# Optimization experiments

Hardware: AMD Instinct MI355X
Metric: run time of the kernel (lower is better)

## Reference

```python
import jax, jax.numpy as jnp
import numpy as np
import math

MODEL_DIM = 1024
BATCH = 4
SEQ = 2048


def setup_inputs() -> dict:
    key = jax.random.key(0)
    kx, kq, kk, kv = jax.random.split(key, 4)
    x = jax.random.normal(kx, (BATCH, SEQ, MODEL_DIM), dtype=jnp.float32)
    # kaiming_uniform_(W.T, a=sqrt(5)) on a square matrix -> U(-b, b) with
    # b = sqrt(6 / ((1 + 5) * fan_in)) = 1/sqrt(model_dim)
    bound = 1.0 / math.sqrt(MODEL_DIM)
    Q = jax.random.uniform(kq, (MODEL_DIM, MODEL_DIM), jnp.float32, -bound, bound)
    K = jax.random.uniform(kk, (MODEL_DIM, MODEL_DIM), jnp.float32, -bound, bound)
    V = jax.random.uniform(kv, (MODEL_DIM, MODEL_DIM), jnp.float32, -bound, bound)
    # attention_input='both' => a = model_dim => F is the full identity mask
    F = jnp.eye(MODEL_DIM, dtype=jnp.float32)
    return {"x": x, "F": F, "Q": Q, "K": K, "V": V}


def reference(x, F, Q, K, V):
    # Qx = x @ F @ Q ; Kx = x @ F @ K ; Vx = x @ V
    xF = x @ F                      # [b, s, d]
    Qx = xF @ Q                     # [b, s, d]
    Kx = xF @ K                     # [b, s, d]
    Vx = x @ V                      # [b, s, d]
    scale = 1.0 / math.sqrt(MODEL_DIM)
    attn_scores = jnp.einsum('bsd,btd->bst', Qx, Kx) * scale  # [b, s, s]
    attn_probs = jax.nn.softmax(attn_scores, axis=-1)
    out = jnp.einsum('bst,btd->bsd', attn_probs, Vx)          # [b, s, d]
    return out
```

## Files before the change

kernel.cpp:

```cpp
#include <hip/hip_runtime.h>
#include <hip/hip_bf16.h>

using bf16 = __hip_bfloat16;
typedef __bf16 bf16x8 __attribute__((ext_vector_type(8)));
typedef float f32x4 __attribute__((ext_vector_type(4)));
typedef float f32x16 __attribute__((ext_vector_type(16)));

#define AS3(p) ((__attribute__((address_space(3))) void*)(p))
#define AS1(p) ((const __attribute__((address_space(1))) void*)(p))

template <int W> __device__ __forceinline__ void waitv() {
  asm volatile("s_waitcnt vmcnt(%0)" ::"n"(W) : "memory");
}
#define BARR __builtin_amdgcn_s_barrier()
#define LGKM0 asm volatile("s_waitcnt lgkmcnt(0)" ::: "memory")
#define SCHEDB __builtin_amdgcn_sched_barrier(0)

__device__ __forceinline__ void swz_bid(int& bx, int& by, int& bz) {
  const int gx = gridDim.x, gy = gridDim.y;
  const int nwg = gx * gy * gridDim.z;
  const int l = blockIdx.x + gx * (blockIdx.y + gy * blockIdx.z);
  const int L = (l & 7) * (nwg >> 3) + (l >> 3);
  bx = L % gx;
  by = (L / gx) % gy;
  bz = L / (gx * gy);
}

__global__ void cast_f32_bf16_kernel(const float* __restrict__ in,
                                     bf16* __restrict__ out, int n4) {
  int i = blockIdx.x * blockDim.x + threadIdx.x;
  if (i >= n4) return;
  float4 v = reinterpret_cast<const float4*>(in)[i];
  union { ushort4 u; bf16 h[4]; } o;
  o.h[0] = __float2bfloat16(v.x);
  o.h[1] = __float2bfloat16(v.y);
  o.h[2] = __float2bfloat16(v.z);
  o.h[3] = __float2bfloat16(v.w);
  reinterpret_cast<ushort4*>(out)[i] = o.u;
}

__global__ void transpose3_kernel(const float* __restrict__ W0,
                                  const float* __restrict__ W1,
                                  const float* __restrict__ W2,
                                  bf16* __restrict__ out) {
  __shared__ bf16 tile[32][33];
  const float* in = (blockIdx.z == 0) ? W0 : (blockIdx.z == 1) ? W1 : W2;
  out += (long)blockIdx.z * 1024 * 1024;
  int c0 = blockIdx.x * 32, r0 = blockIdx.y * 32;
  for (int i = threadIdx.y; i < 32; i += 8)
    tile[i][threadIdx.x] = (bf16)in[(long)(r0 + i) * 1024 + c0 + threadIdx.x];
  __syncthreads();
  for (int i = threadIdx.y; i < 32; i += 8)
    out[(long)(c0 + i) * 1024 + r0 + threadIdx.x] = tile[threadIdx.x][i];
}

__device__ inline void store_c(float* p, float v) { *p = v; }
__device__ inline void store_c(bf16* p, float v) { *p = __float2bfloat16(v); }

template <int MODE, typename OutT>
__global__ __launch_bounds__(512, 1) void gemm8p_kernel(
    const bf16* __restrict__ A, const bf16* __restrict__ Bt, OutT* __restrict__ C,
    int K, int lda, int ldb, int ldc, long sAb, long sBb, long sCb,
    float* __restrict__ aux, int auxStride) {
  constexpr int HALF = 128 * 64;
  constexpr int BB = 4 * HALF;
  __shared__ alignas(16) bf16 lds[2 * BB];

  int bx, by, bz;
  swz_bid(bx, by, bz);
  A += (long)bz * sAb;
  Bt += (long)bz * sBb;
  C += (long)bz * sCb;
  if (MODE != 0) aux += (long)bz * auxStride;
  const int tm = by * 256, tn = bx * 256;
  const int tid = threadIdx.x, wv = tid >> 6, lane = tid & 63;
  const int wm = wv >> 2, wn = wv & 3;
  const int lrow = lane & 15, lkc = lane >> 4;

  f32x4 acc[8][4] = {};
  bf16x8 afr[4][2], bfr[2][2][2];

  const int co0 = (lkc ^ (lrow & 7)) * 8;
  const int co1 = ((4 + lkc) ^ (lrow & 7)) * 8;
  const int arow = wm * 64 + lrow;
  const int brow = wn * 32 + lrow;

  auto stageA = [&](bf16* buf, int kt, int mh) {
#pragma unroll
    for (int i = 0; i < 2; ++i) {
      int slot = i * 512 + tid;
      int rp = slot >> 3;
      int g = (rp & 63) | (mh << 6) | ((rp >> 6) << 7);
      int cg = (slot & 7) ^ (rp & 7);
      const bf16* src = A + (long)(tm + g) * lda + kt + cg * 8;
      __builtin_amdgcn_global_load_lds(AS1(src), AS3(buf + mh * HALF + slot * 8), 16, 0, 0);
    }
  };
  auto stageB = [&](bf16* buf, int kt, int nh) {
#pragma unroll
    for (int i = 0; i < 2; ++i) {
      int slot = i * 512 + tid;
      int rp = slot >> 3;
      int g = (rp & 31) | (nh << 5) | ((rp >> 5) << 6);
      int cg = (slot & 7) ^ (rp & 7);
      const bf16* src = Bt + (long)(tn + g) * ldb + kt + cg * 8;
      __builtin_amdgcn_global_load_lds(AS1(src),
                                       AS3(buf + 2 * HALF + nh * HALF + slot * 8), 16, 0, 0);
    }
  };

#define READ_A(MH)                                                          \
  {                                                                         \
    const bf16* pa = cur + (MH) * HALF;                                     \
    _Pragma("unroll") for (int mi = 0; mi < 4; ++mi) {                      \
      afr[mi][0] = *reinterpret_cast<const bf16x8*>(pa + (arow + mi * 16) * 64 + co0); \
      afr[mi][1] = *reinterpret_cast<const bf16x8*>(pa + (arow + mi * 16) * 64 + co1); \
    }                                                                       \
  }
#define READ_B(NH)                                                          \
  {                                                                         \
    const bf16* pb = cur + 2 * HALF + (NH) * HALF;                          \
    _Pragma("unroll") for (int nj = 0; nj < 2; ++nj) {                      \
      bfr[NH][nj][0] = *reinterpret_cast<const bf16x8*>(pb + (brow + nj * 16) * 64 + co0); \
      bfr[NH][nj][1] = *reinterpret_cast<const bf16x8*>(pb + (brow + nj * 16) * 64 + co1); \
    }                                                                       \
  }
#define MFMA_PH(MH, NH)                                                     \
  __builtin_amdgcn_s_setprio(1);                                            \
  _Pragma("unroll") for (int k = 0; k < 2; ++k)                             \
      _Pragma("unroll") for (int mi = 0; mi < 4; ++mi)                      \
          _Pragma("unroll") for (int nj = 0; nj < 2; ++nj)                  \
    acc[(MH) * 4 + mi][(NH) * 2 + nj] =                                     \
        __builtin_amdgcn_mfma_f32_16x16x32_bf16(                            \
            afr[mi][k], bfr[NH][nj][k], acc[(MH) * 4 + mi][(NH) * 2 + nj],  \
            0, 0, 0);                                                       \
  __builtin_amdgcn_s_setprio(0);

  const int NT = K / 64;
  stageA(lds, 0, 0); stageB(lds, 0, 0);
  stageA(lds, 0, 1); stageB(lds, 0, 1);
  stageA(lds + BB, 64, 0); stageB(lds + BB, 64, 0);
  waitv<8>();
  BARR;

  for (int t = 0; t < NT; ++t) {
    const bf16* cur = lds + (t & 1) * BB;
    bf16* nxt = lds + ((t & 1) ^ 1) * BB;
    READ_A(0) READ_B(0)
    SCHEDB;
    if (t + 1 < NT) { stageA(nxt, (t + 1) * 64, 1); waitv<6>(); }
    else waitv<0>();
    BARR; LGKM0; SCHEDB;
    MFMA_PH(0, 0)
    SCHEDB; BARR;
    READ_B(1)
    SCHEDB;
    if (t + 1 < NT) stageB(nxt, (t + 1) * 64, 1);
    BARR; LGKM0; SCHEDB;
    MFMA_PH(0, 1)
    SCHEDB; BARR;
    READ_A(1)
    SCHEDB;
    if (t + 2 < NT) stageA(nxt == lds ? (bf16*)lds + BB : (bf16*)lds, (t + 2) * 64, 0);
    BARR; LGKM0; SCHEDB;
    MFMA_PH(1, 0)
    SCHEDB; BARR;
    if (t + 2 < NT) {
      stageB(nxt == lds ? (bf16*)lds + BB : (bf16*)lds, (t + 2) * 64, 0);
      waitv<8>();
    } else if (t + 1 < NT) {
      waitv<4>();
    }
    BARR; SCHEDB;
    MFMA_PH(1, 1)
    SCHEDB; BARR;
  }
#undef READ_A
#undef READ_B
#undef MFMA_PH

  const int crow = lkc * 4;
#pragma unroll
  for (int mh = 0; mh < 2; ++mh)
#pragma unroll
    for (int mi = 0; mi < 4; ++mi)
#pragma unroll
      for (int r = 0; r < 4; ++r) {
        const int rowm = tm + wm * 128 + mh * 64 + mi * 16 + crow + r;
        OutT* cp = C + (long)rowm * ldc + tn + wn * 64 + lrow;
        if (MODE == 0) {
#pragma unroll
          for (int nh = 0; nh < 2; ++nh)
#pragma unroll
            for (int nj = 0; nj < 2; ++nj)
              store_c(cp + nh * 32 + nj * 16, acc[mh * 4 + mi][nh * 2 + nj][r]);
        } else {
          float rs = 0.f;
#pragma unroll
          for (int nh = 0; nh < 2; ++nh)
#pragma unroll
            for (int nj = 0; nj < 2; ++nj) {
              float e = __expf(acc[mh * 4 + mi][nh * 2 + nj][r] * 0.03125f);
              rs += e;
              store_c(cp + nh * 32 + nj * 16, e);
            }
          rs += __shfl_xor(rs, 1);
          rs += __shfl_xor(rs, 2);
          rs += __shfl_xor(rs, 4);
          rs += __shfl_xor(rs, 8);
          if ((lane & 15) == 0) atomicAdd(aux + rowm, rs);
        }
      }
}

template <int MODE, typename OutT>
__global__ __launch_bounds__(512, 1) void gemm2p32_kernel(
    const bf16* __restrict__ A, const bf16* __restrict__ Bt, OutT* __restrict__ C,
    int K, int lda, int ldb, int ldc, long sAb, long sBb, long sCb,
    const float* __restrict__ aux, int auxStride) {
  constexpr int BM = 256, BN = 128, BK = 64;
  constexpr int NLA = 4, NLB = 2, NL = 6;
  constexpr int BUFELEM = (BM + BN) * BK;
  __shared__ alignas(16) bf16 lds[2 * BUFELEM];

  int bx, by, bz;
  swz_bid(bx, by, bz);
  A += (long)bz * sAb;
  Bt += (long)bz * sBb;
  C += (long)bz * sCb;
  if (MODE != 0) aux += (long)bz * auxStride;
  const int tm = by * BM, tn = bx * BN;
  const int tid = threadIdx.x, wv = tid >> 6, lane = tid & 63;
  const int wm = wv >> 2, wn = wv & 3;
  const int lcol = lane & 31, khalf = lane >> 5;

  f32x16 acc[4] = {};

  auto stage = [&](int buf, int kt) {
    bf16* base = lds + buf * BUFELEM;
#pragma unroll
    for (int i = 0; i < NLA; ++i) {
      int slot = i * 512 + tid;
      int row = slot >> 3;
      int cg = (slot & 7) ^ (row & 7);
      const bf16* src = A + (long)(tm + row) * lda + kt + cg * 8;
      __builtin_amdgcn_global_load_lds(AS1(src), AS3(base + slot * 8), 16, 0, 0);
    }
#pragma unroll
    for (int i = 0; i < NLB; ++i) {
      int slot = i * 512 + tid;
      int row = slot >> 3;
      int cg = (slot & 7) ^ (row & 7);
      const bf16* src = Bt + (long)(tn + row) * ldb + kt + cg * 8;
      __builtin_amdgcn_global_load_lds(AS1(src), AS3(base + BM * BK + slot * 8), 16, 0, 0);
    }
  };

  const int arow0 = wm * 128 + lcol;
  const int brow = wn * 32 + lcol;

  stage(0, 0);
  const int NT = K / BK;
  for (int t = 0; t < NT; ++t) {
    const int cur = t & 1;
    if (t + 1 < NT) {
      stage(cur ^ 1, (t + 1) * BK);
      waitv<NL>();
    } else {
      waitv<0>();
    }
    BARR;
    SCHEDB;

    const bf16* bA = lds + cur * BUFELEM;
    const bf16* bB = bA + BM * BK;

    bf16x8 bfr[4];
#pragma unroll
    for (int kk = 0; kk < 4; ++kk) {
      int cx = (kk * 2 + khalf) ^ (brow & 7);
      bfr[kk] = *reinterpret_cast<const bf16x8*>(bB + brow * 64 + cx * 8);
    }
#pragma unroll
    for (int ph = 0; ph < 2; ++ph) {
      bf16x8 afr[4][2];
#pragma unroll
      for (int mi = 0; mi < 4; ++mi)
#pragma unroll
        for (int j = 0; j < 2; ++j) {
          int ra = arow0 + mi * 32;
          int cx = ((ph * 2 + j) * 2 + khalf) ^ (ra & 7);
          afr[mi][j] = *reinterpret_cast<const bf16x8*>(bA + ra * 64 + cx * 8);
        }
      __builtin_amdgcn_s_setprio(1);
#pragma unroll
      for (int j = 0; j < 2; ++j)
#pragma unroll
        for (int mi = 0; mi < 4; ++mi)
          acc[mi] = __builtin_amdgcn_mfma_f32_32x32x16_bf16(
              afr[mi][j], bfr[ph * 2 + j], acc[mi], 0, 0, 0);
      __builtin_amdgcn_s_setprio(0);
      SCHEDB;
      BARR;
      SCHEDB;
    }
  }

#pragma unroll
  for (int mi = 0; mi < 4; ++mi)
#pragma unroll
    for (int r = 0; r < 16; ++r) {
      const int row = (r & 3) + 8 * (r >> 2) + 4 * khalf;
      const int rowm = tm + wm * 128 + mi * 32 + row;
      OutT* cp = C + (long)rowm * ldc + tn + wn * 32 + lcol;
      float v = acc[mi][r];
      if (MODE == 2) v *= 1.0f / aux[rowm];
      store_c(cp, v);
    }
}

extern "C" void kernel_launch(void* const* d_in, const int* in_sizes, int n_in,
                              void* d_out, int out_size, void* d_ws, size_t ws_size,
                              hipStream_t stream) {
  const float* x = (const float*)d_in[0];
  const float* Wq = (const float*)d_in[2];
  const float* Wk = (const float*)d_in[3];
  const float* Wv = (const float*)d_in[4];
  float* out = (float*)d_out;

  const long D = 1024, S = 2048, B = 4, MS = B * S;

  bf16* xb  = (bf16*)d_ws;
  bf16* Wtc = xb + MS * D;
  bf16* QKx = Wtc + 3 * D * D;
  bf16* Vxt = QKx + MS * 2 * D;
  bf16* Sc  = Vxt + MS * D;
  float* rowsum = (float*)(Sc + B * S * S);

  dim3 blk(256);
  dim3 tblk(32, 8);

  cast_f32_bf16_kernel<<<(int)(MS * D / 4 / 256), blk, 0, stream>>>(x, xb, (int)(MS * D / 4));
  transpose3_kernel<<<dim3(32, 32, 3), tblk, 0, stream>>>(Wq, Wk, Wv, Wtc);
  gemm8p_kernel<0, bf16><<<dim3(8, 32, 1), 512, 0, stream>>>(
      xb, Wtc, QKx, 1024, 1024, 1024, 2048, 0, 0, 0, nullptr, 0);
  gemm2p32_kernel<0, bf16><<<dim3(16, 4, 4), 512, 0, stream>>>(
      Wtc + 2 * D * D, xb, Vxt, 1024, 1024, 1024, 2048, 0, S * D, D * S, nullptr, 0);
  hipMemsetAsync(rowsum, 0, B * S * sizeof(float), stream);
  gemm8p_kernel<1, bf16><<<dim3(8, 8, 4), 512, 0, stream>>>(
      QKx, QKx + D, Sc, 1024, 2048, 2048, 2048, S * 2 * D, S * 2 * D, S * S,
      rowsum, (int)S);
  gemm2p32_kernel<2, float><<<dim3(8, 8, 4), 512, 0, stream>>>(
      Sc, Vxt, out, 2048, 2048, 2048, 1024, S * S, D * S, S * D,
      rowsum, (int)S);
}
```

Baseline: 173.0 us.

## Restructure gemm8p pipeline to single-tile prefetch; switch gemm2p to 16x16 MFMA

The 8-phase GEMM pipeline is reworked so it prefetches only the next k-tile, spread across the four MFMA phases, with fewer barriers and vmcnt waits per iteration. The 2-phase GEMM moves from a 4x2 wave grid using 32x32x16 MFMA to a 4x2 grid of 64x64 wave tiles using 16x16x32 MFMA, and its epilogue now computes the row-scale reciprocal once per row. The aim is to cut barrier and synchronisation overhead and to change the fragment and LDS read pattern. The trade-off is a shallower prefetch, which may expose more memory latency, and 16x16 MFMAs with a different register footprint.

Measured after the change: 159.8 us. -7.7%, faster.

```diff
diff --git a/kernel.cpp b/kernel.cpp
--- a/kernel.cpp
+++ b/kernel.cpp
@@ -4,7 +4,6 @@
 using bf16 = __hip_bfloat16;
 typedef __bf16 bf16x8 __attribute__((ext_vector_type(8)));
 typedef float f32x4 __attribute__((ext_vector_type(4)));
-typedef float f32x16 __attribute__((ext_vector_type(16)));
 
 #define AS3(p) ((__attribute__((address_space(3))) void*)(p))
 #define AS1(p) ((const __attribute__((address_space(1))) void*)(p))
@@ -137,43 +136,36 @@
   __builtin_amdgcn_s_setprio(0);
 
   const int NT = K / 64;
-  stageA(lds, 0, 0); stageB(lds, 0, 0);
-  stageA(lds, 0, 1); stageB(lds, 0, 1);
-  stageA(lds + BB, 64, 0); stageB(lds + BB, 64, 0);
-  waitv<8>();
-  BARR;
+  stageA(lds, 0, 0);
+  stageB(lds, 0, 0);
+  stageB(lds, 0, 1);
+  stageA(lds, 0, 1);
+  waitv<4>();
+  BARR; SCHEDB;
 
   for (int t = 0; t < NT; ++t) {
     const bf16* cur = lds + (t & 1) * BB;
     bf16* nxt = lds + ((t & 1) ^ 1) * BB;
+    const bool pf = (t + 1 < NT);
+    const int kt1 = (t + 1) * 64;
     READ_A(0) READ_B(0)
-    SCHEDB;
-    if (t + 1 < NT) { stageA(nxt, (t + 1) * 64, 1); waitv<6>(); }
-    else waitv<0>();
-    BARR; LGKM0; SCHEDB;
+    if (pf) stageA(nxt, kt1, 0);
+    LGKM0; SCHEDB;
     MFMA_PH(0, 0)
-    SCHEDB; BARR;
+    if (pf) waitv<2>(); else waitv<0>();
+    BARR; SCHEDB;
     READ_B(1)
-    SCHEDB;
-    if (t + 1 < NT) stageB(nxt, (t + 1) * 64, 1);
-    BARR; LGKM0; SCHEDB;
+    if (pf) stageB(nxt, kt1, 0);
+    LGKM0; SCHEDB;
     MFMA_PH(0, 1)
-    SCHEDB; BARR;
     READ_A(1)
-    SCHEDB;
-    if (t + 2 < NT) stageA(nxt == lds ? (bf16*)lds + BB : (bf16*)lds, (t + 2) * 64, 0);
-    BARR; LGKM0; SCHEDB;
+    if (pf) stageB(nxt, kt1, 1);
+    LGKM0; SCHEDB;
     MFMA_PH(1, 0)
-    SCHEDB; BARR;
-    if (t + 2 < NT) {
-      stageB(nxt == lds ? (bf16*)lds + BB : (bf16*)lds, (t + 2) * 64, 0);
-      waitv<8>();
-    } else if (t + 1 < NT) {
-      waitv<4>();
-    }
+    if (pf) stageA(nxt, kt1, 1);
+    MFMA_PH(1, 1)
+    if (pf) waitv<4>(); else waitv<0>();
     BARR; SCHEDB;
-    MFMA_PH(1, 1)
-    SCHEDB; BARR;
   }
 #undef READ_A
 #undef READ_B
@@ -214,7 +206,7 @@
 }
 
 template <int MODE, typename OutT>
-__global__ __launch_bounds__(512, 1) void gemm2p32_kernel(
+__global__ __launch_bounds__(512, 1) void gemm2p_kernel(
     const bf16* __restrict__ A, const bf16* __restrict__ Bt, OutT* __restrict__ C,
     int K, int lda, int ldb, int ldc, long sAb, long sBb, long sCb,
     const float* __restrict__ aux, int auxStride) {
@@ -231,10 +223,11 @@
   if (MODE != 0) aux += (long)bz * auxStride;
   const int tm = by * BM, tn = bx * BN;
   const int tid = threadIdx.x, wv = tid >> 6, lane = tid & 63;
-  const int wm = wv >> 2, wn = wv & 3;
-  const int lcol = lane & 31, khalf = lane >> 5;
-
-  f32x16 acc[4] = {};
+  const int wm = wv >> 1, wn = wv & 1;
+  const int r0 = wm * 64, c0 = wn * 64;
+  const int lrow = lane & 15, lkc = lane >> 4;
+
+  f32x4 acc[4][4] = {};
 
   auto stage = [&](int buf, int kt) {
     bf16* base = lds + buf * BUFELEM;
@@ -255,9 +248,6 @@
       __builtin_amdgcn_global_load_lds(AS1(src), AS3(base + BM * BK + slot * 8), 16, 0, 0);
     }
   };
-
-  const int arow0 = wm * 128 + lcol;
-  const int brow = wn * 32 + lcol;
 
   stage(0, 0);
   const int NT = K / BK;
@@ -275,30 +265,35 @@
     const bf16* bA = lds + cur * BUFELEM;
     const bf16* bB = bA + BM * BK;
 
-    bf16x8 bfr[4];
-#pragma unroll
-    for (int kk = 0; kk < 4; ++kk) {
-      int cx = (kk * 2 + khalf) ^ (brow & 7);
-      bfr[kk] = *reinterpret_cast<const bf16x8*>(bB + brow * 64 + cx * 8);
-    }
+    bf16x8 bfr[4][2];
+#pragma unroll
+    for (int nj = 0; nj < 4; ++nj)
+#pragma unroll
+      for (int k = 0; k < 2; ++k) {
+        int row = c0 + nj * 16 + lrow;
+        int cx = (k * 4 + lkc) ^ (row & 7);
+        bfr[nj][k] = *reinterpret_cast<const bf16x8*>(bB + row * 64 + cx * 8);
+      }
 #pragma unroll
     for (int ph = 0; ph < 2; ++ph) {
-      bf16x8 afr[4][2];
-#pragma unroll
-      for (int mi = 0; mi < 4; ++mi)
-#pragma unroll
-        for (int j = 0; j < 2; ++j) {
-          int ra = arow0 + mi * 32;
-          int cx = ((ph * 2 + j) * 2 + khalf) ^ (ra & 7);
-          afr[mi][j] = *reinterpret_cast<const bf16x8*>(bA + ra * 64 + cx * 8);
+      bf16x8 afr[2][2];
+#pragma unroll
+      for (int mi = 0; mi < 2; ++mi)
+#pragma unroll
+        for (int k = 0; k < 2; ++k) {
+          int row = r0 + (ph * 2 + mi) * 16 + lrow;
+          int cx = (k * 4 + lkc) ^ (row & 7);
+          afr[mi][k] = *reinterpret_cast<const bf16x8*>(bA + row * 64 + cx * 8);
         }
       __builtin_amdgcn_s_setprio(1);
 #pragma unroll
-      for (int j = 0; j < 2; ++j)
-#pragma unroll
-        for (int mi = 0; mi < 4; ++mi)
-          acc[mi] = __builtin_amdgcn_mfma_f32_32x32x16_bf16(
-              afr[mi][j], bfr[ph * 2 + j], acc[mi], 0, 0, 0);
+      for (int k = 0; k < 2; ++k)
+#pragma unroll
+        for (int mi = 0; mi < 2; ++mi)
+#pragma unroll
+          for (int nj = 0; nj < 4; ++nj)
+            acc[ph * 2 + mi][nj] = __builtin_amdgcn_mfma_f32_16x16x32_bf16(
+                afr[mi][k], bfr[nj][k], acc[ph * 2 + mi][nj], 0, 0, 0);
       __builtin_amdgcn_s_setprio(0);
       SCHEDB;
       BARR;
@@ -306,17 +301,19 @@
     }
   }
 
-#pragma unroll
-  for (int mi = 0; mi < 4; ++mi)
-#pragma unroll
-    for (int r = 0; r < 16; ++r) {
-      const int row = (r & 3) + 8 * (r >> 2) + 4 * khalf;
-      const int rowm = tm + wm * 128 + mi * 32 + row;
-      OutT* cp = C + (long)rowm * ldc + tn + wn * 32 + lcol;
-      float v = acc[mi][r];
-      if (MODE == 2) v *= 1.0f / aux[rowm];
-      store_c(cp, v);
-    }
+  const int crow = lkc * 4;
+#pragma unroll
+  for (int mi = 0; mi < 4; ++mi) {
+#pragma unroll
+    for (int r = 0; r < 4; ++r) {
+      const int rowm = tm + r0 + mi * 16 + crow + r;
+      OutT* cp = C + (long)rowm * ldc + tn + c0 + lrow;
+      float inv = 1.0f;
+      if (MODE == 2) inv = 1.0f / aux[rowm];
+#pragma unroll
+      for (int nj = 0; nj < 4; ++nj) store_c(cp + nj * 16, acc[mi][nj][r] * inv);
+    }
+  }
 }
 
 extern "C" void kernel_launch(void* const* d_in, const int* in_sizes, int n_in,
@@ -344,13 +341,13 @@
   transpose3_kernel<<<dim3(32, 32, 3), tblk, 0, stream>>>(Wq, Wk, Wv, Wtc);
   gemm8p_kernel<0, bf16><<<dim3(8, 32, 1), 512, 0, stream>>>(
       xb, Wtc, QKx, 1024, 1024, 1024, 2048, 0, 0, 0, nullptr, 0);
-  gemm2p32_kernel<0, bf16><<<dim3(16, 4, 4), 512, 0, stream>>>(
+  gemm2p_kernel<0, bf16><<<dim3(16, 4, 4), 512, 0, stream>>>(
       Wtc + 2 * D * D, xb, Vxt, 1024, 1024, 1024, 2048, 0, S * D, D * S, nullptr, 0);
   hipMemsetAsync(rowsum, 0, B * S * sizeof(float), stream);
   gemm8p_kernel<1, bf16><<<dim3(8, 8, 4), 512, 0, stream>>>(
       QKx, QKx + D, Sc, 1024, 2048, 2048, 2048, S * 2 * D, S * 2 * D, S * S,
       rowsum, (int)S);
-  gemm2p32_kernel<2, float><<<dim3(8, 8, 4), 512, 0, stream>>>(
+  gemm2p_kernel<2, float><<<dim3(8, 8, 4), 512, 0, stream>>>(
       Sc, Vxt, out, 2048, 2048, 2048, 1024, S * S, D * S, S * D,
       rowsum, (int)S);
 }
```
